# Performance work log

Hardware: AMD Instinct MI355X
Metric: run time of the kernel (lower is better)

## Reference

```python
import jax, jax.numpy as jnp
import numpy as np

B, N, D, H = 4, 2048, 1024, 16
HD = D // H  # head_dim = 64


def setup_inputs() -> dict:
    key = jax.random.key(0)
    ks = jax.random.split(key, 7)
    q = jax.random.normal(ks[0], (B, N, D), dtype=jnp.float32)
    k = jax.random.normal(ks[1], (B, N, D), dtype=jnp.float32)
    v = jax.random.normal(ks[2], (B, N, D), dtype=jnp.float32)
    scale = 0.02
    Wq = jax.random.normal(ks[3], (D, D), dtype=jnp.float32) * scale
    Wk = jax.random.normal(ks[4], (D, D), dtype=jnp.float32) * scale
    Wv = jax.random.normal(ks[5], (D, D), dtype=jnp.float32) * scale
    Wo = jax.random.normal(ks[6], (D, D), dtype=jnp.float32) * scale
    return {"q": q, "k": k, "v": v, "Wq": Wq, "Wk": Wk, "Wv": Wv, "Wo": Wo}


def _split_heads(x):
    # b n (h d) -> b h n d
    b, n, d = x.shape
    return x.reshape(b, n, H, HD).transpose(0, 2, 1, 3)


def reference(q, k, v, Wq, Wk, Wv, Wo):
    # nn.Linear(bias=False): y = x @ W.T
    qh = _split_heads(q @ Wq.T)
    kh = _split_heads(k @ Wk.T)
    vh = _split_heads(v @ Wv.T)
    scale = jnp.sqrt(jnp.asarray(HD, dtype=jnp.float32))
    scores = jnp.einsum('bhqd,bhkd->bhqk', qh, kh) / scale  # [B,H,N,N]
    # future (causal) mask: triu(ones, diagonal=1) -> masked_fill(-inf)
    future_mask = jnp.triu(jnp.ones((N, N), dtype=bool), k=1)
    scores = jnp.where(future_mask[None, None, :, :], -jnp.inf, scores)
    attn = jax.nn.softmax(scores, axis=-1)
    out = jnp.einsum('bhqk,bhkd->bhqd', attn, vh)
    # b h n d -> b n (h d)
    out = out.transpose(0, 2, 1, 3).reshape(B, N, D)
    return out @ Wo.T
```

## Files before the change

kernel.cpp:

```cpp
#include <hip/hip_runtime.h>
#include <hip/hip_bf16.h>

#define BATCH 4
#define NSEQ 2048
#define DMODEL 1024
#define NHEAD 16
#define HDIM 64

typedef __attribute__((ext_vector_type(8))) short short8;
typedef __attribute__((ext_vector_type(4))) float f32x4;
typedef __attribute__((ext_vector_type(16))) float f32x16;
typedef __attribute__((ext_vector_type(2))) int int2v;
typedef unsigned short ushort_t;

__device__ __forceinline__ ushort_t f2bf(float f) {
    union { float f; unsigned u; } x; x.f = f;
    unsigned r = x.u + 0x7fffu + ((x.u >> 16) & 1u);
    return (ushort_t)(r >> 16);
}

__device__ __forceinline__ unsigned cvt_pk_bf16(float lo, float hi) {
    unsigned r;
    asm("v_cvt_pk_bf16_f32 %0, %1, %2" : "=v"(r) : "v"(lo), "v"(hi));
    return r;
}

#define GLOAD16(gp, lp) __builtin_amdgcn_global_load_lds(                       \
    (const __attribute__((address_space(1))) unsigned*)(const void*)(gp),       \
    (__attribute__((address_space(3))) unsigned*)(void*)(lp), 16, 0, 0)

__global__ __launch_bounds__(256) void cvt_all(const float* __restrict__ q,
                                               const float* __restrict__ k,
                                               const float* __restrict__ v,
                                               const float* __restrict__ w0,
                                               const float* __restrict__ w1,
                                               const float* __restrict__ w2,
                                               const float* __restrict__ w3,
                                               ushort_t* __restrict__ oqkv,
                                               ushort_t* __restrict__ ow) {
    for (int chunk = blockIdx.x; chunk < 14336; chunk += (int)gridDim.x) {
        const float* in;
        ushort_t* out;
        size_t i;
        if (chunk < 12288) {
            int which = chunk >> 12, lb = chunk & 4095;
            in = (which == 0) ? q : ((which == 1) ? k : v);
            i = ((size_t)lb * 256 + threadIdx.x) * 8;
            out = oqkv + (size_t)which * 8388608;
        } else {
            int wb = chunk - 12288;
            int which = wb >> 9, lb = wb & 511;
            in = (which == 0) ? w0 : ((which == 1) ? w1 : ((which == 2) ? w2 : w3));
            i = ((size_t)lb * 256 + threadIdx.x) * 8;
            out = ow + (size_t)which * 1048576;
        }
        float4 f0 = *(const float4*)(in + i);
        float4 f1 = *(const float4*)(in + i + 4);
        short8 o;
        o[0] = f2bf(f0.x); o[1] = f2bf(f0.y); o[2] = f2bf(f0.z); o[3] = f2bf(f0.w);
        o[4] = f2bf(f1.x); o[5] = f2bf(f1.y); o[6] = f2bf(f1.z); o[7] = f2bf(f1.w);
        *(short8*)(out + i) = o;
    }
}

__device__ __forceinline__ void storeC(float* C, size_t idx, float v) { C[idx] = v; }
__device__ __forceinline__ void storeC(ushort_t* C, size_t idx, float v) { C[idx] = f2bf(v); }

template <typename OutT, int LAYOUT>
__global__ __launch_bounds__(512) void gemm_bt8(const ushort_t* __restrict__ A,
                                                const ushort_t* __restrict__ Bt,
                                                OutT* __restrict__ C,
                                                int M, int N, int K, float alpha) {
    __shared__ ushort_t As[3][256 * 64];
    __shared__ ushort_t Bs[3][128 * 64];

    int tid = threadIdx.x;
    int l = tid & 63, w = tid >> 6;
    int wm = w >> 1, wn = w & 1;
    int lr = l & 15, lk = l >> 4;

    int bid = blockIdx.x;
    int wg = (bid & 7) * 32 + (bid >> 3);
    int nbc = N >> 7;
    int brow = (wg / nbc) << 8;
    int bcol = (wg % nbc) << 7;

    int srow8 = l >> 3;
    int sx = ((l & 7) ^ srow8) * 8;
    const ushort_t* pAsrc = A + (size_t)(brow + w * 32 + srow8) * K + sx;
    const ushort_t* pBsrc = Bt + (size_t)(bcol + w * 16 + srow8) * K + sx;
    const size_t rowK8 = (size_t)8 * K;

    int colx = (lk << 4) ^ ((lr & 7) << 4);
    int abyte = (wm * 64 + lr) * 128 + colx;
    int bbyte = (wn * 64 + lr) * 128 + colx;

    f32x4 acc[4][4] = {};
    const int NT = K >> 6;

#pragma unroll
    for (int c = 0; c < 4; c++) GLOAD16(pAsrc + c * rowK8,      &As[0][(w * 32 + 8 * c) * 64]);
#pragma unroll
    for (int c = 0; c < 2; c++) GLOAD16(pBsrc + c * rowK8,      &Bs[0][(w * 16 + 8 * c) * 64]);
#pragma unroll
    for (int c = 0; c < 4; c++) GLOAD16(pAsrc + c * rowK8 + 64, &As[1][(w * 32 + 8 * c) * 64]);
#pragma unroll
    for (int c = 0; c < 2; c++) GLOAD16(pBsrc + c * rowK8 + 64, &Bs[1][(w * 16 + 8 * c) * 64]);

    int slot = 0, stslot = 2;
    for (int T = 0; T < NT; ++T) {
        if (T < NT - 1) { asm volatile("s_waitcnt vmcnt(6)" ::: "memory"); }
        else            { asm volatile("s_waitcnt vmcnt(0)" ::: "memory"); }
        __builtin_amdgcn_sched_barrier(0);
        __builtin_amdgcn_s_barrier();
        asm volatile("" ::: "memory");

        const char* ab = (const char*)&As[slot][0];
        const char* bb = (const char*)&Bs[slot][0];
        bool stage = (T + 2 < NT);
        int k2 = (T + 2) << 6;

        short8 af[4], bf_[4];
#pragma unroll
        for (int m = 0; m < 4; m++) af[m]  = *(const short8*)(ab + abyte + m * 2048);
#pragma unroll
        for (int n = 0; n < 4; n++) bf_[n] = *(const short8*)(bb + bbyte + n * 2048);
        if (stage) {
            GLOAD16(pAsrc + 0 * rowK8 + k2, &As[stslot][(w * 32 + 0) * 64]);
            GLOAD16(pAsrc + 1 * rowK8 + k2, &As[stslot][(w * 32 + 8) * 64]);
            GLOAD16(pAsrc + 2 * rowK8 + k2, &As[stslot][(w * 32 + 16) * 64]);
        }
        __builtin_amdgcn_s_setprio(1);
#pragma unroll
        for (int m = 0; m < 4; m++)
#pragma unroll
            for (int n = 0; n < 4; n++)
                acc[m][n] = __builtin_amdgcn_mfma_f32_16x16x32_bf16(af[m], bf_[n], acc[m][n], 0, 0, 0);
        __builtin_amdgcn_s_setprio(0);

#pragma unroll
        for (int m = 0; m < 4; m++) af[m]  = *(const short8*)(ab + (abyte ^ 64) + m * 2048);
#pragma unroll
        for (int n = 0; n < 4; n++) bf_[n] = *(const short8*)(bb + (bbyte ^ 64) + n * 2048);
        if (stage) {
            GLOAD16(pAsrc + 3 * rowK8 + k2, &As[stslot][(w * 32 + 24) * 64]);
            GLOAD16(pBsrc + 0 * rowK8 + k2, &Bs[stslot][(w * 16 + 0) * 64]);
            GLOAD16(pBsrc + 1 * rowK8 + k2, &Bs[stslot][(w * 16 + 8) * 64]);
        }
        __builtin_amdgcn_s_setprio(1);
#pragma unroll
        for (int m = 0; m < 4; m++)
#pragma unroll
            for (int n = 0; n < 4; n++)
                acc[m][n] = __builtin_amdgcn_mfma_f32_16x16x32_bf16(af[m], bf_[n], acc[m][n], 0, 0, 0);
        __builtin_amdgcn_s_setprio(0);

        slot = (slot == 2) ? 0 : slot + 1;
        stslot = (stslot == 2) ? 0 : stslot + 1;
    }

#pragma unroll
    for (int m = 0; m < 4; m++)
#pragma unroll
        for (int n = 0; n < 4; n++)
#pragma unroll
            for (int r = 0; r < 4; r++) {
                int row = brow + wm * 64 + m * 16 + lk * 4 + r;
                int col = bcol + wn * 64 + n * 16 + lr;
                float v = acc[m][n][r] * alpha;
                if (LAYOUT == 0) {
                    storeC(C, (size_t)row * N + col, v);
                } else if (LAYOUT == 1) {
                    int b = row >> 11, nn = row & 2047, h = col >> 6, d = col & 63;
                    size_t idx = ((size_t)(b * NHEAD + h) << 17) + ((size_t)(nn >> 5) << 11) +
                                 ((d >> 4) << 9) + ((nn & 31) << 4) + (d & 15);
                    storeC(C, idx, v);
                } else {
                    int b = row >> 11, kk = row & 2047, h = col >> 6, d = col & 63;
                    size_t idx = ((size_t)(b * NHEAD + h) << 17) + ((size_t)(kk >> 6) << 12) +
                                 ((d >> 5) << 11) + (((kk >> 4) & 3) << 9) + ((d & 31) << 4) + (kk & 15);
                    storeC(C, idx, v);
                }
            }
}

__device__ __forceinline__ void pack_pfr(const f32x16& S0, const f32x16& S1, short8 (&pfr)[4]) {
    unsigned pw0[8], pw1[8];
#pragma unroll
    for (int jj = 0; jj < 8; jj++) {
        pw0[jj] = cvt_pk_bf16(S0[2 * jj], S0[2 * jj + 1]);
        pw1[jj] = cvt_pk_bf16(S1[2 * jj], S1[2 * jj + 1]);
    }
    union U { unsigned u[4]; short8 s; };
    int2v a, bb;
    a  = __builtin_amdgcn_permlane32_swap((int)pw0[0], (int)pw0[2], false, false);
    bb = __builtin_amdgcn_permlane32_swap((int)pw0[1], (int)pw0[3], false, false);
    U u0; u0.u[0] = (unsigned)a[0]; u0.u[1] = (unsigned)bb[0];
          u0.u[2] = (unsigned)a[1]; u0.u[3] = (unsigned)bb[1];
    pfr[0] = u0.s;
    a  = __builtin_amdgcn_permlane32_swap((int)pw0[4], (int)pw0[6], false, false);
    bb = __builtin_amdgcn_permlane32_swap((int)pw0[5], (int)pw0[7], false, false);
    U u1; u1.u[0] = (unsigned)a[0]; u1.u[1] = (unsigned)bb[0];
          u1.u[2] = (unsigned)a[1]; u1.u[3] = (unsigned)bb[1];
    pfr[1] = u1.s;
    a  = __builtin_amdgcn_permlane32_swap((int)pw1[0], (int)pw1[2], false, false);
    bb = __builtin_amdgcn_permlane32_swap((int)pw1[1], (int)pw1[3], false, false);
    U u2; u2.u[0] = (unsigned)a[0]; u2.u[1] = (unsigned)bb[0];
          u2.u[2] = (unsigned)a[1]; u2.u[3] = (unsigned)bb[1];
    pfr[2] = u2.s;
    a  = __builtin_amdgcn_permlane32_swap((int)pw1[4], (int)pw1[6], false, false);
    bb = __builtin_amdgcn_permlane32_swap((int)pw1[5], (int)pw1[7], false, false);
    U u3; u3.u[0] = (unsigned)a[0]; u3.u[1] = (unsigned)bb[0];
          u3.u[2] = (unsigned)a[1]; u3.u[3] = (unsigned)bb[1];
    pfr[3] = u3.s;
}

__global__ __launch_bounds__(256, 2) void attn_kernel(const ushort_t* __restrict__ Qp,
                                                      const ushort_t* __restrict__ Kp,
                                                      const ushort_t* __restrict__ VT,
                                                      ushort_t* __restrict__ AO) {
    int tid = threadIdx.x;
    int l = tid & 63, w = tid >> 6;
    int lq = l & 31;
    int hi = l >> 5;
    int bid = blockIdx.x;
    int x = bid & 7, jj = bid >> 3;
    int bh = x + 8 * (jj & 7);
    int pi = (jj >> 3) * 4 + w;
    int qiL = pi, qiH = 63 - pi;
    int jlo = (qiL >> 1) + 1;
    int jhi = (qiH >> 1) + 1;
    int b = bh >> 4;

    const size_t hb = (size_t)bh << 17;
    const size_t base = ((size_t)b * NSEQ) * DMODEL + (size_t)(bh & 15) * HDIM;

    int qgL = qiL * 32 + lq;
    int qgH = qiH * 32 + lq;
    int loff = lq * 16 + 8 * hi;

    const ushort_t* kpbase = Kp + hb + loff;
    const ushort_t* vpbase = VT + hb + loff;

    short8 qfL[4], qfH[4];
    {
        const ushort_t* qpL = Qp + hb + ((size_t)qiL << 11) + loff;
        const ushort_t* qpH = Qp + hb + ((size_t)qiH << 11) + loff;
#pragma unroll
        for (int c = 0; c < 4; c++) { qfL[c] = *(const short8*)(qpL + (c << 9));
                                      qfH[c] = *(const short8*)(qpH + (c << 9)); }
    }

    f32x16 OL0 = {}, OL1 = {}, OH0 = {}, OH1 = {};
    float lrunL = 0.f, lrunH = 0.f;

    short8 kA0[4], kA1[4], kB0[4], kB1[4];
#pragma unroll
    for (int c = 0; c < 4; c++) { kA0[c] = *(const short8*)(kpbase + (c << 9));
                                  kA1[c] = *(const short8*)(kpbase + 2048 + (c << 9)); }

#define ATTN_STEP(kc0, kc1, kn0, kn1, J, PREF) do {                              \
        int j_ = (J); int k0_ = j_ << 6;                                         \
        short8 vf0[4], vf1[4];                                                   \
        { const ushort_t* vp = vpbase + ((size_t)j_ << 12);                      \
          _Pragma("unroll")                                                      \
          for (int c = 0; c < 4; c++) { vf0[c] = *(const short8*)(vp + (c << 9));\
                                        vf1[c] = *(const short8*)(vp + 2048 + (c << 9)); } } \
                                                   \
        f32x16 S0 = {}, S1 = {};                                                 \
        _Pragma("unroll")                                                        \
        for (int c = 0; c < 4; c++) { S0 = __builtin_amdgcn_mfma_f32_32x32x16_bf16(kc0[c], qfH[c], S0, 0, 0, 0); } \
        _Pragma("unroll")                                                        \
        for (int c = 0; c < 4; c++) { S1 = __builtin_amdgcn_mfma_f32_32x32x16_bf16(kc1[c], qfH[c], S1, 0, 0, 0); } \
        if (j_ == jhi - 1) {                                                     \
            _Pragma("unroll")                                                    \
            for (int r = 0; r < 16; r++) {                                       \
                int kk = k0_ + (r & 3) + 8 * (r >> 2) + 4 * hi;                  \
                if (kk > qgH)      S0[r] = -1e30f;                               \
                if (kk + 32 > qgH) S1[r] = -1e30f;                               \
            }                                                                    \
        }                                                                        \
        float rsH = 0.f;                                                         \
        _Pragma("unroll")                                                        \
        for (int r = 0; r < 16; r++) {                                           \
            S0[r] = __builtin_amdgcn_exp2f(S0[r] - 32.f);                        \
            S1[r] = __builtin_amdgcn_exp2f(S1[r] - 32.f);                        \
            rsH += S0[r] + S1[r];                                                \
        }                                                                        \
        rsH += __shfl_xor(rsH, 32);                                              \
        lrunH += rsH;                                                            \
        short8 pfrH[4];                                                          \
        pack_pfr(S0, S1, pfrH);                                                  \
                                                      \
        bool actL = (j_ < jlo);                                                  \
        if (actL) {                                                              \
            S0 = (f32x16){}; S1 = (f32x16){};                                    \
            _Pragma("unroll")                                                    \
            for (int c = 0; c < 4; c++) { S0 = __builtin_amdgcn_mfma_f32_32x32x16_bf16(kc0[c], qfL[c], S0, 0, 0, 0); } \
            _Pragma("unroll")                                                    \
            for (int c = 0; c < 4; c++) { S1 = __builtin_amdgcn_mfma_f32_32x32x16_bf16(kc1[c], qfL[c], S1, 0, 0, 0); } \
        }                                                                        \
                                              \
        if (PREF) {                                                              \
            const ushort_t* kp = kpbase + ((size_t)(2 * (j_ + 1)) << 11);        \
            _Pragma("unroll")                                                    \
            for (int c = 0; c < 4; c++) { kn0[c] = *(const short8*)(kp + (c << 9)); \
                                          kn1[c] = *(const short8*)(kp + 2048 + (c << 9)); } \
        }                                                                        \
                                                                       \
        _Pragma("unroll")                                                        \
        for (int c = 0; c < 4; c++) { OH0 = __builtin_amdgcn_mfma_f32_32x32x16_bf16(vf0[c], pfrH[c], OH0, 0, 0, 0); } \
        _Pragma("unroll")                                                        \
        for (int c = 0; c < 4; c++) { OH1 = __builtin_amdgcn_mfma_f32_32x32x16_bf16(vf1[c], pfrH[c], OH1, 0, 0, 0); } \
                                                   \
        if (actL) {                                                              \
            if (j_ == jlo - 1) {                                                 \
                _Pragma("unroll")                                                \
                for (int r = 0; r < 16; r++) {                                   \
                    int kk = k0_ + (r & 3) + 8 * (r >> 2) + 4 * hi;              \
                    if (kk > qgL)      S0[r] = -1e30f;                           \
                    if (kk + 32 > qgL) S1[r] = -1e30f;                           \
                }                                                                \
            }                                                                    \
            float rsL = 0.f;                                                     \
            _Pragma("unroll")                                                    \
            for (int r = 0; r < 16; r++) {                                       \
                S0[r] = __builtin_amdgcn_exp2f(S0[r] - 32.f);                    \
                S1[r] = __builtin_amdgcn_exp2f(S1[r] - 32.f);                    \
                rsL += S0[r] + S1[r];                                            \
            }                                                                    \
            rsL += __shfl_xor(rsL, 32);                                          \
            lrunL += rsL;                                                        \
            short8 pfrL[4];                                                      \
            pack_pfr(S0, S1, pfrL);                                              \
            _Pragma("unroll")                                                    \
            for (int c = 0; c < 4; c++) { OL0 = __builtin_amdgcn_mfma_f32_32x32x16_bf16(vf0[c], pfrL[c], OL0, 0, 0, 0); } \
            _Pragma("unroll")                                                    \
            for (int c = 0; c < 4; c++) { OL1 = __builtin_amdgcn_mfma_f32_32x32x16_bf16(vf1[c], pfrL[c], OL1, 0, 0, 0); } \
        }                                                                        \
    } while (0)

    int j = 0;
    for (; j + 1 < jhi; j += 2) {
        ATTN_STEP(kA0, kA1, kB0, kB1, j, true);
        ATTN_STEP(kB0, kB1, kA0, kA1, j + 1, (j + 2 < jhi));
    }
    if (j < jhi) ATTN_STEP(kA0, kA1, kB0, kB1, j, false);
#undef ATTN_STEP

    {
        float inv = 1.f / lrunL;
        size_t rowoff = base + (size_t)qgL * DMODEL;
#pragma unroll
        for (int q4 = 0; q4 < 4; q4++) {
            uint2 ua = {cvt_pk_bf16(OL0[4 * q4] * inv,     OL0[4 * q4 + 1] * inv),
                        cvt_pk_bf16(OL0[4 * q4 + 2] * inv, OL0[4 * q4 + 3] * inv)};
            *(uint2*)(AO + rowoff + 8 * q4 + 4 * hi) = ua;
            uint2 ub = {cvt_pk_bf16(OL1[4 * q4] * inv,     OL1[4 * q4 + 1] * inv),
                        cvt_pk_bf16(OL1[4 * q4 + 2] * inv, OL1[4 * q4 + 3] * inv)};
            *(uint2*)(AO + rowoff + 32 + 8 * q4 + 4 * hi) = ub;
        }
    }
    {
        float inv = 1.f / lrunH;
        size_t rowoff = base + (size_t)qgH * DMODEL;
#pragma unroll
        for (int q4 = 0; q4 < 4; q4++) {
            uint2 ua = {cvt_pk_bf16(OH0[4 * q4] * inv,     OH0[4 * q4 + 1] * inv),
                        cvt_pk_bf16(OH0[4 * q4 + 2] * inv, OH0[4 * q4 + 3] * inv)};
            *(uint2*)(AO + rowoff + 8 * q4 + 4 * hi) = ua;
            uint2 ub = {cvt_pk_bf16(OH1[4 * q4] * inv,     OH1[4 * q4 + 1] * inv),
                        cvt_pk_bf16(OH1[4 * q4 + 2] * inv, OH1[4 * q4 + 3] * inv)};
            *(uint2*)(AO + rowoff + 32 + 8 * q4 + 4 * hi) = ub;
        }
    }
}

extern "C" void kernel_launch(void* const* d_in, const int* in_sizes, int n_in,
                              void* d_out, int out_size, void* d_ws, size_t ws_size,
                              hipStream_t stream) {
    const float* q  = (const float*)d_in[0];
    const float* k  = (const float*)d_in[1];
    const float* v  = (const float*)d_in[2];
    const float* Wq = (const float*)d_in[3];
    const float* Wk = (const float*)d_in[4];
    const float* Wv = (const float*)d_in[5];
    const float* Wo = (const float*)d_in[6];
    float* out = (float*)d_out;

    const size_t BND = (size_t)BATCH * NSEQ * DMODEL;
    const size_t WSZ = (size_t)DMODEL * DMODEL;
    const size_t need = (7 * BND + 4 * WSZ) * sizeof(ushort_t);
    if (ws_size < need) return;

    ushort_t* ws  = (ushort_t*)d_ws;
    ushort_t* qb  = ws;
    ushort_t* kb  = qb + BND;
    ushort_t* vb  = kb + BND;
    ushort_t* Qp  = vb + BND;
    ushort_t* Kp  = Qp + BND;
    ushort_t* VT  = Kp + BND;
    ushort_t* AO  = VT + BND;
    ushort_t* Wqb = AO + BND;

    const int M = BATCH * NSEQ;

    cvt_all<<<2048, 256, 0, stream>>>(q, k, v, Wq, Wk, Wv, Wo, qb, Wqb);

    int gblocks = (M / 256) * (DMODEL / 128);
    gemm_bt8<ushort_t, 1><<<gblocks, 512, 0, stream>>>(qb, Wqb, Qp, M, DMODEL, DMODEL, 0.18033688011112043f);
    gemm_bt8<ushort_t, 1><<<gblocks, 512, 0, stream>>>(kb, Wqb + WSZ, Kp, M, DMODEL, DMODEL, 1.0f);
    gemm_bt8<ushort_t, 2><<<gblocks, 512, 0, stream>>>(vb, Wqb + 2 * WSZ, VT, M, DMODEL, DMODEL, 1.0f);

    attn_kernel<<<512, 256, 0, stream>>>(Qp, Kp, VT, AO);

    gemm_bt8<float, 0><<<gblocks, 512, 0, stream>>>(AO, Wqb + 3 * WSZ, out, M, DMODEL, DMODEL, 1.0f);
}
```

Measured before the change: 167.8 us.

## Fuse Q/K/V projection GEMMs into one launch and fold softmax offset into MFMA init

Merges the three projection GEMM launches into a single 768-block kernel that picks its input, weight, output layout and scale from the block index, so the three fill one grid and pay launch and tail costs once. In the attention kernel, the constant -32 exp2 offset now seeds the score accumulators instead of being subtracted per element. Row sums are split into two accumulators to shorten the dependency chain. The output GEMM is specialised to fp32 row-major with no alpha multiply. The fused kernel adds runtime selects on the layout in the epilogue.

```diff
diff --git a/kernel.cpp b/kernel.cpp
--- a/kernel.cpp
+++ b/kernel.cpp
@@ -23,6 +23,11 @@
     unsigned r;
     asm("v_cvt_pk_bf16_f32 %0, %1, %2" : "=v"(r) : "v"(lo), "v"(hi));
     return r;
+}
+
+__device__ __forceinline__ f32x16 splat16(float x) {
+    f32x16 v = {};
+    return v + x;
 }
 
 #define GLOAD16(gp, lp) __builtin_amdgcn_global_load_lds(                       \
@@ -66,11 +71,133 @@
 __device__ __forceinline__ void storeC(float* C, size_t idx, float v) { C[idx] = v; }
 __device__ __forceinline__ void storeC(ushort_t* C, size_t idx, float v) { C[idx] = f2bf(v); }
 
-template <typename OutT, int LAYOUT>
-__global__ __launch_bounds__(512) void gemm_bt8(const ushort_t* __restrict__ A,
+#define GEMM_CORE(As, Bs, pAsrc, pBsrc, rowK8, NT, acc, abyte, bbyte, w)         \
+    do {                                                                         \
+        _Pragma("unroll")                                                        \
+        for (int c = 0; c < 4; c++) GLOAD16(pAsrc + c * rowK8,      &As[0][(w * 32 + 8 * c) * 64]); \
+        _Pragma("unroll")                                                        \
+        for (int c = 0; c < 2; c++) GLOAD16(pBsrc + c * rowK8,      &Bs[0][(w * 16 + 8 * c) * 64]); \
+        _Pragma("unroll")                                                        \
+        for (int c = 0; c < 4; c++) GLOAD16(pAsrc + c * rowK8 + 64, &As[1][(w * 32 + 8 * c) * 64]); \
+        _Pragma("unroll")                                                        \
+        for (int c = 0; c < 2; c++) GLOAD16(pBsrc + c * rowK8 + 64, &Bs[1][(w * 16 + 8 * c) * 64]); \
+        int slot = 0, stslot = 2;                                                \
+        for (int T = 0; T < NT; ++T) {                                           \
+            if (T < NT - 1) { asm volatile("s_waitcnt vmcnt(6)" ::: "memory"); } \
+            else            { asm volatile("s_waitcnt vmcnt(0)" ::: "memory"); } \
+            __builtin_amdgcn_sched_barrier(0);                                   \
+            __builtin_amdgcn_s_barrier();                                        \
+            asm volatile("" ::: "memory");                                       \
+            const char* ab = (const char*)&As[slot][0];                          \
+            const char* bb = (const char*)&Bs[slot][0];                          \
+            bool stage = (T + 2 < NT);                                           \
+            int k2 = (T + 2) << 6;                                               \
+            short8 af[4], bf_[4];                                                \
+            _Pragma("unroll")                                                    \
+            for (int m = 0; m < 4; m++) af[m]  = *(const short8*)(ab + abyte + m * 2048); \
+            _Pragma("unroll")                                                    \
+            for (int n = 0; n < 4; n++) bf_[n] = *(const short8*)(bb + bbyte + n * 2048); \
+            if (stage) {                                                         \
+                GLOAD16(pAsrc + 0 * rowK8 + k2, &As[stslot][(w * 32 + 0) * 64]); \
+                GLOAD16(pAsrc + 1 * rowK8 + k2, &As[stslot][(w * 32 + 8) * 64]); \
+                GLOAD16(pAsrc + 2 * rowK8 + k2, &As[stslot][(w * 32 + 16) * 64]);\
+            }                                                                    \
+            __builtin_amdgcn_s_setprio(1);                                       \
+            _Pragma("unroll")                                                    \
+            for (int m = 0; m < 4; m++)                                          \
+                _Pragma("unroll")                                                \
+                for (int n = 0; n < 4; n++)                                      \
+                    acc[m][n] = __builtin_amdgcn_mfma_f32_16x16x32_bf16(af[m], bf_[n], acc[m][n], 0, 0, 0); \
+            __builtin_amdgcn_s_setprio(0);                                       \
+            _Pragma("unroll")                                                    \
+            for (int m = 0; m < 4; m++) af[m]  = *(const short8*)(ab + (abyte ^ 64) + m * 2048); \
+            _Pragma("unroll")                                                    \
+            for (int n = 0; n < 4; n++) bf_[n] = *(const short8*)(bb + (bbyte ^ 64) + n * 2048); \
+            if (stage) {                                                         \
+                GLOAD16(pAsrc + 3 * rowK8 + k2, &As[stslot][(w * 32 + 24) * 64]);\
+                GLOAD16(pBsrc + 0 * rowK8 + k2, &Bs[stslot][(w * 16 + 0) * 64]); \
+                GLOAD16(pBsrc + 1 * rowK8 + k2, &Bs[stslot][(w * 16 + 8) * 64]); \
+            }                                                                    \
+            __builtin_amdgcn_s_setprio(1);                                       \
+            _Pragma("unroll")                                                    \
+            for (int m = 0; m < 4; m++)                                          \
+                _Pragma("unroll")                                                \
+                for (int n = 0; n < 4; n++)                                      \
+                    acc[m][n] = __builtin_amdgcn_mfma_f32_16x16x32_bf16(af[m], bf_[n], acc[m][n], 0, 0, 0); \
+            __builtin_amdgcn_s_setprio(0);                                       \
+            slot = (slot == 2) ? 0 : slot + 1;                                   \
+            stslot = (stslot == 2) ? 0 : stslot + 1;                             \
+        }                                                                        \
+    } while (0)
+
+__global__ __launch_bounds__(512) void proj_gemm(const ushort_t* __restrict__ qb,
+                                                 const ushort_t* __restrict__ kb,
+                                                 const ushort_t* __restrict__ vb,
+                                                 const ushort_t* __restrict__ W4,
+                                                 ushort_t* __restrict__ Qp,
+                                                 ushort_t* __restrict__ Kp,
+                                                 ushort_t* __restrict__ VTp) {
+    __shared__ ushort_t As[3][256 * 64];
+    __shared__ ushort_t Bs[3][128 * 64];
+
+    const int K = DMODEL;
+    int sel = blockIdx.x >> 8;
+    const ushort_t* A  = (sel == 0) ? qb : ((sel == 1) ? kb : vb);
+    const ushort_t* Bt = W4 + (size_t)sel * (DMODEL * DMODEL);
+    ushort_t* C = (sel == 0) ? Qp : ((sel == 1) ? Kp : VTp);
+    float alpha = (sel == 0) ? 0.18033688011112043f : 1.0f;
+
+    int tid = threadIdx.x;
+    int l = tid & 63, w = tid >> 6;
+    int wm = w >> 1, wn = w & 1;
+    int lr = l & 15, lk = l >> 4;
+
+    int bid = blockIdx.x & 255;
+    int wg = (bid & 7) * 32 + (bid >> 3);
+    int brow = (wg >> 3) << 8;
+    int bcol = (wg & 7) << 7;
+
+    int srow8 = l >> 3;
+    int sx = ((l & 7) ^ srow8) * 8;
+    const ushort_t* pAsrc = A + (size_t)(brow + w * 32 + srow8) * K + sx;
+    const ushort_t* pBsrc = Bt + (size_t)(bcol + w * 16 + srow8) * K + sx;
+    const size_t rowK8 = (size_t)8 * K;
+
+    int colx = (lk << 4) ^ ((lr & 7) << 4);
+    int abyte = (wm * 64 + lr) * 128 + colx;
+    int bbyte = (wn * 64 + lr) * 128 + colx;
+
+    f32x4 acc[4][4] = {};
+    const int NT = K >> 6;
+
+    GEMM_CORE(As, Bs, pAsrc, pBsrc, rowK8, NT, acc, abyte, bbyte, w);
+
+#pragma unroll
+    for (int m = 0; m < 4; m++)
+#pragma unroll
+        for (int n = 0; n < 4; n++)
+#pragma unroll
+            for (int r = 0; r < 4; r++) {
+                int row = brow + wm * 64 + m * 16 + lk * 4 + r;
+                int col = bcol + wn * 64 + n * 16 + lr;
+                float v = acc[m][n][r] * alpha;
+                int b = row >> 11, nn = row & 2047, h = col >> 6, d = col & 63;
+                size_t idx;
+                if (sel != 2) {
+                    idx = ((size_t)(b * NHEAD + h) << 17) + ((size_t)(nn >> 5) << 11) +
+                          ((d >> 4) << 9) + ((nn & 31) << 4) + (d & 15);
+                } else {
+                    idx = ((size_t)(b * NHEAD + h) << 17) + ((size_t)(nn >> 6) << 12) +
+                          ((d >> 5) << 11) + (((nn >> 4) & 3) << 9) + ((d & 31) << 4) + (nn & 15);
+                }
+                C[idx] = f2bf(v);
+            }
+}
+
+__global__ __launch_bounds__(512) void out_gemm(const ushort_t* __restrict__ A,
                                                 const ushort_t* __restrict__ Bt,
-                                                OutT* __restrict__ C,
-                                                int M, int N, int K, float alpha) {
+                                                float* __restrict__ C,
+                                                int M, int N, int K) {
     __shared__ ushort_t As[3][256 * 64];
     __shared__ ushort_t Bs[3][128 * 64];
 
@@ -98,66 +225,7 @@
     f32x4 acc[4][4] = {};
     const int NT = K >> 6;
 
-#pragma unroll
-    for (int c = 0; c < 4; c++) GLOAD16(pAsrc + c * rowK8,      &As[0][(w * 32 + 8 * c) * 64]);
-#pragma unroll
-    for (int c = 0; c < 2; c++) GLOAD16(pBsrc + c * rowK8,      &Bs[0][(w * 16 + 8 * c) * 64]);
-#pragma unroll
-    for (int c = 0; c < 4; c++) GLOAD16(pAsrc + c * rowK8 + 64, &As[1][(w * 32 + 8 * c) * 64]);
-#pragma unroll
-    for (int c = 0; c < 2; c++) GLOAD16(pBsrc + c * rowK8 + 64, &Bs[1][(w * 16 + 8 * c) * 64]);
-
-    int slot = 0, stslot = 2;
-    for (int T = 0; T < NT; ++T) {
-        if (T < NT - 1) { asm volatile("s_waitcnt vmcnt(6)" ::: "memory"); }
-        else            { asm volatile("s_waitcnt vmcnt(0)" ::: "memory"); }
-        __builtin_amdgcn_sched_barrier(0);
-        __builtin_amdgcn_s_barrier();
-        asm volatile("" ::: "memory");
-
-        const char* ab = (const char*)&As[slot][0];
-        const char* bb = (const char*)&Bs[slot][0];
-        bool stage = (T + 2 < NT);
-        int k2 = (T + 2) << 6;
-
-        short8 af[4], bf_[4];
-#pragma unroll
-        for (int m = 0; m < 4; m++) af[m]  = *(const short8*)(ab + abyte + m * 2048);
-#pragma unroll
-        for (int n = 0; n < 4; n++) bf_[n] = *(const short8*)(bb + bbyte + n * 2048);
-        if (stage) {
-            GLOAD16(pAsrc + 0 * rowK8 + k2, &As[stslot][(w * 32 + 0) * 64]);
-            GLOAD16(pAsrc + 1 * rowK8 + k2, &As[stslot][(w * 32 + 8) * 64]);
-            GLOAD16(pAsrc + 2 * rowK8 + k2, &As[stslot][(w * 32 + 16) * 64]);
-        }
-        __builtin_amdgcn_s_setprio(1);
-#pragma unroll
-        for (int m = 0; m < 4; m++)
-#pragma unroll
-            for (int n = 0; n < 4; n++)
-                acc[m][n] = __builtin_amdgcn_mfma_f32_16x16x32_bf16(af[m], bf_[n], acc[m][n], 0, 0, 0);
-        __builtin_amdgcn_s_setprio(0);
-
-#pragma unroll
-        for (int m = 0; m < 4; m++) af[m]  = *(const short8*)(ab + (abyte ^ 64) + m * 2048);
-#pragma unroll
-        for (int n = 0; n < 4; n++) bf_[n] = *(const short8*)(bb + (bbyte ^ 64) + n * 2048);
-        if (stage) {
-            GLOAD16(pAsrc + 3 * rowK8 + k2, &As[stslot][(w * 32 + 24) * 64]);
-            GLOAD16(pBsrc + 0 * rowK8 + k2, &Bs[stslot][(w * 16 + 0) * 64]);
-            GLOAD16(pBsrc + 1 * rowK8 + k2, &Bs[stslot][(w * 16 + 8) * 64]);
-        }
-        __builtin_amdgcn_s_setprio(1);
-#pragma unroll
-        for (int m = 0; m < 4; m++)
-#pragma unroll
-            for (int n = 0; n < 4; n++)
-                acc[m][n] = __builtin_amdgcn_mfma_f32_16x16x32_bf16(af[m], bf_[n], acc[m][n], 0, 0, 0);
-        __builtin_amdgcn_s_setprio(0);
-
-        slot = (slot == 2) ? 0 : slot + 1;
-        stslot = (stslot == 2) ? 0 : stslot + 1;
-    }
+    GEMM_CORE(As, Bs, pAsrc, pBsrc, rowK8, NT, acc, abyte, bbyte, w);
 
 #pragma unroll
     for (int m = 0; m < 4; m++)
@@ -167,20 +235,7 @@
             for (int r = 0; r < 4; r++) {
                 int row = brow + wm * 64 + m * 16 + lk * 4 + r;
                 int col = bcol + wn * 64 + n * 16 + lr;
-                float v = acc[m][n][r] * alpha;
-                if (LAYOUT == 0) {
-                    storeC(C, (size_t)row * N + col, v);
-                } else if (LAYOUT == 1) {
-                    int b = row >> 11, nn = row & 2047, h = col >> 6, d = col & 63;
-                    size_t idx = ((size_t)(b * NHEAD + h) << 17) + ((size_t)(nn >> 5) << 11) +
-                                 ((d >> 4) << 9) + ((nn & 31) << 4) + (d & 15);
-                    storeC(C, idx, v);
-                } else {
-                    int b = row >> 11, kk = row & 2047, h = col >> 6, d = col & 63;
-                    size_t idx = ((size_t)(b * NHEAD + h) << 17) + ((size_t)(kk >> 6) << 12) +
-                                 ((d >> 5) << 11) + (((kk >> 4) & 3) << 9) + ((d & 31) << 4) + (kk & 15);
-                    storeC(C, idx, v);
-                }
+                C[(size_t)row * N + col] = acc[m][n][r];
             }
 }
 
@@ -266,8 +321,8 @@
           _Pragma("unroll")                                                      \
           for (int c = 0; c < 4; c++) { vf0[c] = *(const short8*)(vp + (c << 9));\
                                         vf1[c] = *(const short8*)(vp + 2048 + (c << 9)); } } \
-                                                   \
-        f32x16 S0 = {}, S1 = {};                                                 \
+                \
+        f32x16 S0 = splat16(-32.f), S1 = splat16(-32.f);                         \
         _Pragma("unroll")                                                        \
         for (int c = 0; c < 4; c++) { S0 = __builtin_amdgcn_mfma_f32_32x32x16_bf16(kc0[c], qfH[c], S0, 0, 0, 0); } \
         _Pragma("unroll")                                                        \
@@ -280,13 +335,14 @@
                 if (kk + 32 > qgH) S1[r] = -1e30f;                               \
             }                                                                    \
         }                                                                        \
-        float rsH = 0.f;                                                         \
+        float rsHa = 0.f, rsHb = 0.f;                                            \
         _Pragma("unroll")                                                        \
         for (int r = 0; r < 16; r++) {                                           \
-            S0[r] = __builtin_amdgcn_exp2f(S0[r] - 32.f);                        \
-            S1[r] = __builtin_amdgcn_exp2f(S1[r] - 32.f);                        \
-            rsH += S0[r] + S1[r];                                                \
-        }                                                                        \
+            S0[r] = __builtin_amdgcn_exp2f(S0[r]);                               \
+            S1[r] = __builtin_amdgcn_exp2f(S1[r]);                               \
+            rsHa += S0[r]; rsHb += S1[r];                                        \
+        }                                                                        \
+        float rsH = rsHa + rsHb;                                                 \
         rsH += __shfl_xor(rsH, 32);                                              \
         lrunH += rsH;                                                            \
         short8 pfrH[4];                                                          \
@@ -294,7 +350,7 @@
                                                       \
         bool actL = (j_ < jlo);                                                  \
         if (actL) {                                                              \
-            S0 = (f32x16){}; S1 = (f32x16){};                                    \
+            S0 = splat16(-32.f); S1 = splat16(-32.f);                            \
             _Pragma("unroll")                                                    \
             for (int c = 0; c < 4; c++) { S0 = __builtin_amdgcn_mfma_f32_32x32x16_bf16(kc0[c], qfL[c], S0, 0, 0, 0); } \
             _Pragma("unroll")                                                    \
@@ -322,13 +378,14 @@
                     if (kk + 32 > qgL) S1[r] = -1e30f;                           \
                 }                                                                \
             }                                                                    \
-            float rsL = 0.f;                                                     \
+            float rsLa = 0.f, rsLb = 0.f;                                        \
             _Pragma("unroll")                                                    \
             for (int r = 0; r < 16; r++) {                                       \
-                S0[r] = __builtin_amdgcn_exp2f(S0[r] - 32.f);                    \
-                S1[r] = __builtin_amdgcn_exp2f(S1[r] - 32.f);                    \
-                rsL += S0[r] + S1[r];                                            \
+                S0[r] = __builtin_amdgcn_exp2f(S0[r]);                           \
+                S1[r] = __builtin_amdgcn_exp2f(S1[r]);                           \
+                rsLa += S0[r]; rsLb += S1[r];                                    \
             }                                                                    \
+            float rsL = rsLa + rsLb;                                             \
             rsL += __shfl_xor(rsL, 32);                                          \
             lrunL += rsL;                                                        \
             short8 pfrL[4];                                                      \
@@ -407,12 +464,9 @@
 
     cvt_all<<<2048, 256, 0, stream>>>(q, k, v, Wq, Wk, Wv, Wo, qb, Wqb);
 
-    int gblocks = (M / 256) * (DMODEL / 128);
-    gemm_bt8<ushort_t, 1><<<gblocks, 512, 0, stream>>>(qb, Wqb, Qp, M, DMODEL, DMODEL, 0.18033688011112043f);
-    gemm_bt8<ushort_t, 1><<<gblocks, 512, 0, stream>>>(kb, Wqb + WSZ, Kp, M, DMODEL, DMODEL, 1.0f);
-    gemm_bt8<ushort_t, 2><<<gblocks, 512, 0, stream>>>(vb, Wqb + 2 * WSZ, VT, M, DMODEL, DMODEL, 1.0f);
+    proj_gemm<<<768, 512, 0, stream>>>(qb, kb, vb, Wqb, Qp, Kp, VT);
 
     attn_kernel<<<512, 256, 0, stream>>>(Qp, Kp, VT, AO);
 
-    gemm_bt8<float, 0><<<gblocks, 512, 0, stream>>>(AO, Wqb + 3 * WSZ, out, M, DMODEL, DMODEL, 1.0f);
-}
+    out_gemm<<<256, 512, 0, stream>>>(AO, Wqb + 3 * WSZ, out, M, DMODEL, DMODEL);
+}
```

Measured after the change: 183.3 us. +9.2%, slower.

## Shrink GEMM tile to 128x128 with 4 waves, double buffering, and raise MFMA priority in attention

Applied to the files above, without the earlier changes.

The projection GEMMs move from a 256x128 tile with 8 waves and a triple-buffered LDS pipeline to a 128x128 tile with 4 waves, double buffering, two blocks per CU, and twice as many blocks. This aims to raise occupancy and wave count across CUs and to cut LDS per block. In exchange it waits for all loads (vmcnt(0)) each iteration, so there is less load/compute overlap, and each B tile is reused less. The attention kernel also wraps its MFMA groups in s_setprio(1) so matrix work gets issue priority over other waves.

```diff
diff --git a/kernel.cpp b/kernel.cpp
--- a/kernel.cpp
+++ b/kernel.cpp
@@ -67,12 +67,12 @@
 __device__ __forceinline__ void storeC(ushort_t* C, size_t idx, float v) { C[idx] = f2bf(v); }
 
 template <typename OutT, int LAYOUT>
-__global__ __launch_bounds__(512) void gemm_bt8(const ushort_t* __restrict__ A,
-                                                const ushort_t* __restrict__ Bt,
-                                                OutT* __restrict__ C,
-                                                int M, int N, int K, float alpha) {
-    __shared__ ushort_t As[3][256 * 64];
-    __shared__ ushort_t Bs[3][128 * 64];
+__global__ __launch_bounds__(256, 2) void gemm_bt8(const ushort_t* __restrict__ A,
+                                                   const ushort_t* __restrict__ Bt,
+                                                   OutT* __restrict__ C,
+                                                   int M, int N, int K, float alpha) {
+    __shared__ ushort_t As[2][128 * 64];
+    __shared__ ushort_t Bs[2][128 * 64];
 
     int tid = threadIdx.x;
     int l = tid & 63, w = tid >> 6;
@@ -80,15 +80,15 @@
     int lr = l & 15, lk = l >> 4;
 
     int bid = blockIdx.x;
-    int wg = (bid & 7) * 32 + (bid >> 3);
+    int wg = (bid & 7) * ((int)gridDim.x >> 3) + (bid >> 3);
     int nbc = N >> 7;
-    int brow = (wg / nbc) << 8;
+    int brow = (wg / nbc) << 7;
     int bcol = (wg % nbc) << 7;
 
     int srow8 = l >> 3;
     int sx = ((l & 7) ^ srow8) * 8;
     const ushort_t* pAsrc = A + (size_t)(brow + w * 32 + srow8) * K + sx;
-    const ushort_t* pBsrc = Bt + (size_t)(bcol + w * 16 + srow8) * K + sx;
+    const ushort_t* pBsrc = Bt + (size_t)(bcol + w * 32 + srow8) * K + sx;
     const size_t rowK8 = (size_t)8 * K;
 
     int colx = (lk << 4) ^ ((lr & 7) << 4);
@@ -99,26 +99,22 @@
     const int NT = K >> 6;
 
 #pragma unroll
-    for (int c = 0; c < 4; c++) GLOAD16(pAsrc + c * rowK8,      &As[0][(w * 32 + 8 * c) * 64]);
-#pragma unroll
-    for (int c = 0; c < 2; c++) GLOAD16(pBsrc + c * rowK8,      &Bs[0][(w * 16 + 8 * c) * 64]);
-#pragma unroll
-    for (int c = 0; c < 4; c++) GLOAD16(pAsrc + c * rowK8 + 64, &As[1][(w * 32 + 8 * c) * 64]);
-#pragma unroll
-    for (int c = 0; c < 2; c++) GLOAD16(pBsrc + c * rowK8 + 64, &Bs[1][(w * 16 + 8 * c) * 64]);
-
-    int slot = 0, stslot = 2;
+    for (int c = 0; c < 4; c++) GLOAD16(pAsrc + c * rowK8, &As[0][(w * 32 + 8 * c) * 64]);
+#pragma unroll
+    for (int c = 0; c < 4; c++) GLOAD16(pBsrc + c * rowK8, &Bs[0][(w * 32 + 8 * c) * 64]);
+
+    int slot = 0;
     for (int T = 0; T < NT; ++T) {
-        if (T < NT - 1) { asm volatile("s_waitcnt vmcnt(6)" ::: "memory"); }
-        else            { asm volatile("s_waitcnt vmcnt(0)" ::: "memory"); }
+        asm volatile("s_waitcnt vmcnt(0)" ::: "memory");
         __builtin_amdgcn_sched_barrier(0);
         __builtin_amdgcn_s_barrier();
         asm volatile("" ::: "memory");
 
         const char* ab = (const char*)&As[slot][0];
         const char* bb = (const char*)&Bs[slot][0];
-        bool stage = (T + 2 < NT);
-        int k2 = (T + 2) << 6;
+        int ns = slot ^ 1;
+        bool stage = (T + 1 < NT);
+        int k1 = (T + 1) << 6;
 
         short8 af[4], bf_[4];
 #pragma unroll
@@ -126,9 +122,10 @@
 #pragma unroll
         for (int n = 0; n < 4; n++) bf_[n] = *(const short8*)(bb + bbyte + n * 2048);
         if (stage) {
-            GLOAD16(pAsrc + 0 * rowK8 + k2, &As[stslot][(w * 32 + 0) * 64]);
-            GLOAD16(pAsrc + 1 * rowK8 + k2, &As[stslot][(w * 32 + 8) * 64]);
-            GLOAD16(pAsrc + 2 * rowK8 + k2, &As[stslot][(w * 32 + 16) * 64]);
+            GLOAD16(pAsrc + 0 * rowK8 + k1, &As[ns][(w * 32 + 0) * 64]);
+            GLOAD16(pAsrc + 1 * rowK8 + k1, &As[ns][(w * 32 + 8) * 64]);
+            GLOAD16(pAsrc + 2 * rowK8 + k1, &As[ns][(w * 32 + 16) * 64]);
+            GLOAD16(pAsrc + 3 * rowK8 + k1, &As[ns][(w * 32 + 24) * 64]);
         }
         __builtin_amdgcn_s_setprio(1);
 #pragma unroll
@@ -143,9 +140,10 @@
 #pragma unroll
         for (int n = 0; n < 4; n++) bf_[n] = *(const short8*)(bb + (bbyte ^ 64) + n * 2048);
         if (stage) {
-            GLOAD16(pAsrc + 3 * rowK8 + k2, &As[stslot][(w * 32 + 24) * 64]);
-            GLOAD16(pBsrc + 0 * rowK8 + k2, &Bs[stslot][(w * 16 + 0) * 64]);
-            GLOAD16(pBsrc + 1 * rowK8 + k2, &Bs[stslot][(w * 16 + 8) * 64]);
+            GLOAD16(pBsrc + 0 * rowK8 + k1, &Bs[ns][(w * 32 + 0) * 64]);
+            GLOAD16(pBsrc + 1 * rowK8 + k1, &Bs[ns][(w * 32 + 8) * 64]);
+            GLOAD16(pBsrc + 2 * rowK8 + k1, &Bs[ns][(w * 32 + 16) * 64]);
+            GLOAD16(pBsrc + 3 * rowK8 + k1, &Bs[ns][(w * 32 + 24) * 64]);
         }
         __builtin_amdgcn_s_setprio(1);
 #pragma unroll
@@ -155,8 +153,7 @@
                 acc[m][n] = __builtin_amdgcn_mfma_f32_16x16x32_bf16(af[m], bf_[n], acc[m][n], 0, 0, 0);
         __builtin_amdgcn_s_setprio(0);
 
-        slot = (slot == 2) ? 0 : slot + 1;
-        stslot = (stslot == 2) ? 0 : stslot + 1;
+        slot ^= 1;
     }
 
 #pragma unroll
@@ -268,10 +265,12 @@
                                         vf1[c] = *(const short8*)(vp + 2048 + (c << 9)); } } \
                                                    \
         f32x16 S0 = {}, S1 = {};                                                 \
+        __builtin_amdgcn_s_setprio(1);                                           \
         _Pragma("unroll")                                                        \
         for (int c = 0; c < 4; c++) { S0 = __builtin_amdgcn_mfma_f32_32x32x16_bf16(kc0[c], qfH[c], S0, 0, 0, 0); } \
         _Pragma("unroll")                                                        \
         for (int c = 0; c < 4; c++) { S1 = __builtin_amdgcn_mfma_f32_32x32x16_bf16(kc1[c], qfH[c], S1, 0, 0, 0); } \
+        __builtin_amdgcn_s_setprio(0);                                           \
         if (j_ == jhi - 1) {                                                     \
             _Pragma("unroll")                                                    \
             for (int r = 0; r < 16; r++) {                                       \
@@ -295,10 +294,12 @@
         bool actL = (j_ < jlo);                                                  \
         if (actL) {                                                              \
             S0 = (f32x16){}; S1 = (f32x16){};                                    \
+            __builtin_amdgcn_s_setprio(1);                                       \
             _Pragma("unroll")                                                    \
             for (int c = 0; c < 4; c++) { S0 = __builtin_amdgcn_mfma_f32_32x32x16_bf16(kc0[c], qfL[c], S0, 0, 0, 0); } \
             _Pragma("unroll")                                                    \
             for (int c = 0; c < 4; c++) { S1 = __builtin_amdgcn_mfma_f32_32x32x16_bf16(kc1[c], qfL[c], S1, 0, 0, 0); } \
+            __builtin_amdgcn_s_setprio(0);                                       \
         }                                                                        \
                                               \
         if (PREF) {                                                              \
@@ -308,10 +309,12 @@
                                           kn1[c] = *(const short8*)(kp + 2048 + (c << 9)); } \
         }                                                                        \
                                                                        \
+        __builtin_amdgcn_s_setprio(1);                                           \
         _Pragma("unroll")                                                        \
         for (int c = 0; c < 4; c++) { OH0 = __builtin_amdgcn_mfma_f32_32x32x16_bf16(vf0[c], pfrH[c], OH0, 0, 0, 0); } \
         _Pragma("unroll")                                                        \
         for (int c = 0; c < 4; c++) { OH1 = __builtin_amdgcn_mfma_f32_32x32x16_bf16(vf1[c], pfrH[c], OH1, 0, 0, 0); } \
+        __builtin_amdgcn_s_setprio(0);                                           \
                                                    \
         if (actL) {                                                              \
             if (j_ == jlo - 1) {                                                 \
@@ -333,10 +336,12 @@
             lrunL += rsL;                                                        \
             short8 pfrL[4];                                                      \
             pack_pfr(S0, S1, pfrL);                                              \
+            __builtin_amdgcn_s_setprio(1);                                       \
             _Pragma("unroll")                                                    \
             for (int c = 0; c < 4; c++) { OL0 = __builtin_amdgcn_mfma_f32_32x32x16_bf16(vf0[c], pfrL[c], OL0, 0, 0, 0); } \
             _Pragma("unroll")                                                    \
             for (int c = 0; c < 4; c++) { OL1 = __builtin_amdgcn_mfma_f32_32x32x16_bf16(vf1[c], pfrL[c], OL1, 0, 0, 0); } \
+            __builtin_amdgcn_s_setprio(0);                                       \
         }                                                                        \
     } while (0)
 
@@ -407,12 +412,12 @@
 
     cvt_all<<<2048, 256, 0, stream>>>(q, k, v, Wq, Wk, Wv, Wo, qb, Wqb);
 
-    int gblocks = (M / 256) * (DMODEL / 128);
-    gemm_bt8<ushort_t, 1><<<gblocks, 512, 0, stream>>>(qb, Wqb, Qp, M, DMODEL, DMODEL, 0.18033688011112043f);
-    gemm_bt8<ushort_t, 1><<<gblocks, 512, 0, stream>>>(kb, Wqb + WSZ, Kp, M, DMODEL, DMODEL, 1.0f);
-    gemm_bt8<ushort_t, 2><<<gblocks, 512, 0, stream>>>(vb, Wqb + 2 * WSZ, VT, M, DMODEL, DMODEL, 1.0f);
+    int gblocks = (M / 128) * (DMODEL / 128);
+    gemm_bt8<ushort_t, 1><<<gblocks, 256, 0, stream>>>(qb, Wqb, Qp, M, DMODEL, DMODEL, 0.18033688011112043f);
+    gemm_bt8<ushort_t, 1><<<gblocks, 256, 0, stream>>>(kb, Wqb + WSZ, Kp, M, DMODEL, DMODEL, 1.0f);
+    gemm_bt8<ushort_t, 2><<<gblocks, 256, 0, stream>>>(vb, Wqb + 2 * WSZ, VT, M, DMODEL, DMODEL, 1.0f);
 
     attn_kernel<<<512, 256, 0, stream>>>(Qp, Kp, VT, AO);
 
-    gemm_bt8<float, 0><<<gblocks, 512, 0, stream>>>(AO, Wqb + 3 * WSZ, out, M, DMODEL, DMODEL, 1.0f);
-}
+    gemm_bt8<float, 0><<<gblocks, 256, 0, stream>>>(AO, Wqb + 3 * WSZ, out, M, DMODEL, DMODEL, 1.0f);
+}
```

New measurement: 171.7 us. 2.3% more time.
